# Kernel tuning notes

Measured on AMD Instinct MI355X. Metric: run time of the kernel, lower is better.

## Reference

```python
import jax, jax.numpy as jnp
import numpy as np

N_NODES = 50000
N_EDGES = 800000
IN_DIM = 128
HID = 128


def setup_inputs() -> dict:
    key = jax.random.key(0)
    ks = jax.random.split(key, 8)
    s = 1.0 / np.sqrt(IN_DIM)
    return {
        "x": jax.random.normal(ks[0], (N_NODES, IN_DIM), dtype=jnp.float32),
        "edge_index": jax.random.randint(ks[1], (2, N_EDGES), 0, N_NODES, dtype=jnp.int32),
        "W1_l": jax.random.uniform(ks[2], (HID, IN_DIM), jnp.float32, -s, s),
        "b1": jnp.zeros((HID,), jnp.float32),
        "W1_r": jax.random.uniform(ks[3], (HID, IN_DIM), jnp.float32, -s, s),
        "W2_l": jax.random.uniform(ks[4], (HID, HID), jnp.float32, -s, s),
        "b2": jnp.zeros((HID,), jnp.float32),
        "W2_r": jax.random.uniform(ks[5], (HID, HID), jnp.float32, -s, s),
    }


def _sage_conv(x, src, dst, W_l, b, W_r, n_nodes):
    # mean aggregation of source features onto destination nodes
    msg = x[src]                                    # [E, d] gather
    agg = jax.ops.segment_sum(msg, dst, num_segments=n_nodes)  # [N, d]
    deg = jax.ops.segment_sum(jnp.ones((src.shape[0],), x.dtype), dst,
                              num_segments=n_nodes)            # [N]
    agg = agg / jnp.maximum(deg, 1.0)[:, None]
    # PyG SAGEConv: lin_l(aggr) + lin_r(x_self), bias in lin_l
    return agg @ W_l.T + b + x @ W_r.T


def reference(x, edge_index, W1_l, b1, W1_r, W2_l, b2, W2_r):
    src, dst = edge_index[0], edge_index[1]
    n = x.shape[0]
    h = jax.nn.relu(_sage_conv(x, src, dst, W1_l, b1, W1_r, n))
    # dropout is identity in eval mode
    out = jax.nn.relu(_sage_conv(h, src, dst, W2_l, b2, W2_r, n))
    return out
```

## Files before the change

kernel.cpp:

```cpp
#include <hip/hip_runtime.h>

#define N_NODES 50000
#define N_EDGES 800000
#define DIM 128
#define NBINS 782
#define CAP 2048
#define EPB 8192
#define NSCAT 98

typedef _Float16 f16;
typedef _Float16 f16x4 __attribute__((ext_vector_type(4)));
typedef _Float16 f16x8 __attribute__((ext_vector_type(8)));
typedef float    f32x2 __attribute__((ext_vector_type(2)));
typedef float    f32x4 __attribute__((ext_vector_type(4)));
typedef unsigned short u16;
typedef unsigned char  u8;

__device__ inline int bucketof(int d) {
    if (d < 10) return 0;
    if (d < 13) return 1;
    if (d < 16) return 2;
    if (d < 19) return 3;
    if (d < 22) return 4;
    if (d < 26) return 5;
    if (d < 32) return 6;
    return 7;
}


__global__ __launch_bounds__(256) void k_prep(const float* __restrict__ x, u8* __restrict__ x8,
                                              const float* __restrict__ W1l, const float* __restrict__ W1r,
                                              const float* __restrict__ W2l, const float* __restrict__ W2r,
                                              f16* __restrict__ Wf1, f16* __restrict__ Wf2,
                                              int* __restrict__ binfill) {
    int b = blockIdx.x;
    if (b < 3125) {
        int idx = b * 256 + threadIdx.x;
        const float* xp = x + (size_t)idx * 8;
        float4 v0 = *(const float4*)xp;
        float4 v1 = *(const float4*)(xp + 4);
        int r0 = 0, r1 = 0;
        r0 = __builtin_amdgcn_cvt_pk_fp8_f32(v0.x, v0.y, r0, false);
        r0 = __builtin_amdgcn_cvt_pk_fp8_f32(v0.z, v0.w, r0, true);
        r1 = __builtin_amdgcn_cvt_pk_fp8_f32(v1.x, v1.y, r1, false);
        r1 = __builtin_amdgcn_cvt_pk_fp8_f32(v1.z, v1.w, r1, true);
        uint2 w; w.x = (unsigned)r0; w.y = (unsigned)r1;
        *(uint2*)(x8 + (size_t)idx * 8) = w;
    } else if (b < 3157) {
        int t = (b - 3125) * 256 + threadIdx.x;
        int layer = t >> 12;
        int nt = (t >> 9) & 7;
        int kk = (t >> 6) & 7;
        int lane = t & 63;
        int r = lane & 15, g = lane >> 4;
        int n = nt * 16 + r;
        const float* Wl_ = layer ? W2l : W1l;
        const float* Wr_ = layer ? W2r : W1r;
        f16x8 frag;
#pragma unroll
        for (int j = 0; j < 8; ++j) {
            int k = kk * 32 + g * 4 + (j & 3) + ((j >> 2) << 4);
            float f = (k < 128) ? Wl_[n * 128 + k] : Wr_[n * 128 + (k - 128)];
            frag[j] = (f16)f;
        }
        f16* dstp = (layer ? Wf2 : Wf1) + ((size_t)((nt * 8 + kk) * 64 + lane)) * 8;
        *(f16x8*)dstp = frag;
    } else {
        for (int i = threadIdx.x; i < NBINS; i += 256) binfill[i] = 0;
    }
}


__global__ __launch_bounds__(1024) void k_binscat(const int* __restrict__ src, const int* __restrict__ dst,
                                                  int* __restrict__ binfill, int* __restrict__ pairs) {
    __shared__ int hist[NBINS];
    __shared__ int base[NBINS];
    int t = threadIdx.x;
    for (int i = t; i < NBINS; i += 1024) hist[i] = 0;
    __syncthreads();
    int e0 = blockIdx.x * EPB;
    int mybin[8], myrank[8], mypack[8];
#pragma unroll
    for (int j = 0; j < 8; ++j) {
        int e = e0 + j * 1024 + t;
        if (e < N_EDGES) {
            int d = dst[e];
            int bin = d >> 6;
            mybin[j] = bin;
            mypack[j] = (src[e] << 6) | (d & 63);
            myrank[j] = atomicAdd(&hist[bin], 1);
        } else {
            mybin[j] = -1;
        }
    }
    __syncthreads();
    for (int i = t; i < NBINS; i += 1024) base[i] = atomicAdd(&binfill[i], hist[i]);
    __syncthreads();
#pragma unroll
    for (int j = 0; j < 8; ++j) {
        if (mybin[j] >= 0) {
            int bin = mybin[j];
            int pos = base[bin] + myrank[j];
            if (pos < CAP) pairs[bin * CAP + pos] = mypack[j];
        }
    }
}


__global__ __launch_bounds__(256) void k_binsolve(const int* __restrict__ pairs, const int* __restrict__ binfill,
                                                  u16* __restrict__ srt, int* __restrict__ rowbeg,
                                                  int* __restrict__ degA, int* __restrict__ order) {
    __shared__ int lcnt[64];
    __shared__ int lptr[64];
    __shared__ int lcur[64];
    __shared__ int h8[8];
    __shared__ int bb[8];
    int bin = blockIdx.x;
    int t = threadIdx.x;
    int p0 = bin * CAP;
    int cnt = min(binfill[bin], CAP);
    if (t < 64) lcnt[t] = 0;
    if (t < 8) h8[t] = 0;
    __syncthreads();
    for (int i = t; i < cnt; i += 256) atomicAdd(&lcnt[pairs[p0 + i] & 63], 1);
    __syncthreads();
    if (t < 64) {
        int d = lcnt[t];
        int v = d;
#pragma unroll
        for (int off = 1; off < 64; off <<= 1) {
            int u = __shfl_up(v, off);
            if (t >= off) v += u;
        }
        lptr[t] = v - d;
        lcur[t] = v - d;
    }
    __syncthreads();
    for (int i = t; i < cnt; i += 256) {
        int p = pairs[p0 + i];
        int slot = atomicAdd(&lcur[p & 63], 1);
        srt[p0 + slot] = (u16)(p >> 6);
    }
    int node = bin * 64 + t;
    bool act = (t < 64) && (node < N_NODES);
    int b = 0, r8 = 0;
    if (act) {
        rowbeg[node] = p0 + lptr[t];
        degA[node] = lcnt[t];
        b = bucketof(lcnt[t]);
        r8 = atomicAdd(&h8[b], 1);
    }
    __syncthreads();
    if (t == 0) {
        int r = 0;
#pragma unroll
        for (int i = 0; i < 8; ++i) { bb[i] = r; r += h8[i]; }
    }
    __syncthreads();
    if (act) order[bin * 64 + bb[b] + r8] = node;
}


__global__ __launch_bounds__(256) void k_fused(const u8* __restrict__ X8, const float* __restrict__ Xf,
                                               const f16* __restrict__ Xh16, const u16* __restrict__ srt,
                                               const int* __restrict__ rowbeg, const int* __restrict__ degA,
                                               const int* __restrict__ order, const f16* __restrict__ Wf,
                                               const float* __restrict__ bias,
                                               float* __restrict__ C, f16* __restrict__ Cb16,
                                               u8* __restrict__ Cb8) {
    __shared__ f16 agg[64][136];
    int bin = blockIdx.x;
    int n0 = bin << 6;
    int t = threadIdx.x;
    int g = t >> 4, l16 = t & 15;
    int nvalid = N_NODES - n0; if (nvalid > 64) nvalid = 64;
    const u8* __restrict__ base = X8 + l16 * 8;

#pragma unroll
    for (int p = 0; p < 4; ++p) {
        int rank = p * 16 + g;
        if (rank < nvalid) {
            int node = order[n0 + rank];
            int m = node - n0;
            int beg = rowbeg[node];
            int d = degA[node];
            int end = beg + d;
            f32x2 A0[4], A1[4], A2[4], A3[4];
#pragma unroll
            for (int j = 0; j < 4; ++j) {
                A0[j] = (f32x2){0.f, 0.f}; A1[j] = (f32x2){0.f, 0.f};
                A2[j] = (f32x2){0.f, 0.f}; A3[j] = (f32x2){0.f, 0.f};
            }
            int e = beg;
#define GACC(Ar, w) { Ar[0] += __builtin_amdgcn_cvt_pk_f32_fp8((w).x, false); \
                      Ar[1] += __builtin_amdgcn_cvt_pk_f32_fp8((w).x, true);  \
                      Ar[2] += __builtin_amdgcn_cvt_pk_f32_fp8((w).y, false); \
                      Ar[3] += __builtin_amdgcn_cvt_pk_f32_fp8((w).y, true); }
            for (; e + 4 <= end; e += 4) {
                int s0 = __builtin_nontemporal_load(srt + e);
                int s1 = __builtin_nontemporal_load(srt + e + 1);
                int s2 = __builtin_nontemporal_load(srt + e + 2);
                int s3 = __builtin_nontemporal_load(srt + e + 3);
                uint2 w0 = *(const uint2*)(base + (size_t)s0 * DIM);
                uint2 w1 = *(const uint2*)(base + (size_t)s1 * DIM);
                uint2 w2 = *(const uint2*)(base + (size_t)s2 * DIM);
                uint2 w3 = *(const uint2*)(base + (size_t)s3 * DIM);
                GACC(A0, w0); GACC(A1, w1); GACC(A2, w2); GACC(A3, w3);
            }
            if (e < end)     { uint2 w = *(const uint2*)(base + (size_t)__builtin_nontemporal_load(srt + e) * DIM); GACC(A0, w); }
            if (e + 1 < end) { uint2 w = *(const uint2*)(base + (size_t)__builtin_nontemporal_load(srt + e + 1) * DIM); GACC(A1, w); }
            if (e + 2 < end) { uint2 w = *(const uint2*)(base + (size_t)__builtin_nontemporal_load(srt + e + 2) * DIM); GACC(A2, w); }
#undef GACC
            float inv = 1.0f / fmaxf((float)d, 1.0f);
            f16x8 r;
#pragma unroll
            for (int j = 0; j < 4; ++j) {
                f32x2 s = (A0[j] + A1[j]) + (A2[j] + A3[j]);
                r[j * 2]     = (f16)(s.x * inv);
                r[j * 2 + 1] = (f16)(s.y * inv);
            }
            *(f16x8*)&agg[m][l16 * 8] = r;
        }
    }
    __syncthreads();

    int wave = t >> 6, lane = t & 63;
    int r = lane & 15, gg = lane >> 4;
    int rowloc = wave * 16 + r;
    size_t grow = (size_t)n0 + rowloc;
    size_t growc = (grow < N_NODES) ? grow : (N_NODES - 1);

    f32x4 acc[8];
#pragma unroll
    for (int nt = 0; nt < 8; ++nt) acc[nt] = (f32x4){0.f, 0.f, 0.f, 0.f};

#pragma unroll
    for (int kk = 0; kk < 8; ++kk) {
        f16x8 a;
        if (kk < 4) {
            f16x4 q0 = *(const f16x4*)&agg[rowloc][kk * 32 + gg * 4];
            f16x4 q1 = *(const f16x4*)&agg[rowloc][kk * 32 + gg * 4 + 16];
            a = __builtin_shufflevector(q0, q1, 0, 1, 2, 3, 4, 5, 6, 7);
        } else if (Xf) {
            const float* ar = Xf + growc * DIM + (kk - 4) * 32 + gg * 4;
            float4 u0 = *(const float4*)(ar);
            float4 u1 = *(const float4*)(ar + 16);
            a[0]=(f16)u0.x; a[1]=(f16)u0.y; a[2]=(f16)u0.z; a[3]=(f16)u0.w;
            a[4]=(f16)u1.x; a[5]=(f16)u1.y; a[6]=(f16)u1.z; a[7]=(f16)u1.w;
        } else {
            const f16* ar = Xh16 + growc * DIM + (kk - 4) * 32 + gg * 4;
            f16x4 q0 = *(const f16x4*)(ar);
            f16x4 q1 = *(const f16x4*)(ar + 16);
            a = __builtin_shufflevector(q0, q1, 0, 1, 2, 3, 4, 5, 6, 7);
        }
#pragma unroll
        for (int nt = 0; nt < 8; ++nt) {
            f16x8 b = *(const f16x8*)(Wf + ((size_t)((nt * 8 + kk) * 64 + lane)) * 8);
            acc[nt] = __builtin_amdgcn_mfma_f32_16x16x32_f16(a, b, acc[nt], 0, 0, 0);
        }
    }
    size_t rbase = (size_t)n0 + wave * 16 + gg * 4;
#pragma unroll
    for (int nt = 0; nt < 8; ++nt) {
        int colc = nt * 16 + r;
        float bv = bias[colc];
#pragma unroll
        for (int q = 0; q < 4; ++q) {
            size_t node = rbase + q;
            if (node < N_NODES) {
                float v = fmaxf(acc[nt][q] + bv, 0.f);
                if (C)    C[node * DIM + colc] = v;
                if (Cb16) Cb16[node * DIM + colc] = (f16)v;
                if (Cb8) {
                    int pk = __builtin_amdgcn_cvt_pk_fp8_f32(v, v, 0, false);
                    Cb8[node * DIM + colc] = (u8)(pk & 0xff);
                }
            }
        }
    }
}


extern "C" void kernel_launch(void* const* d_in, const int* in_sizes, int n_in,
                              void* d_out, int out_size, void* d_ws, size_t ws_size,
                              hipStream_t stream) {
    const float* x   = (const float*)d_in[0];
    const int*   ei  = (const int*)d_in[1];
    const float* W1l = (const float*)d_in[2];
    const float* b1  = (const float*)d_in[3];
    const float* W1r = (const float*)d_in[4];
    const float* W2l = (const float*)d_in[5];
    const float* b2  = (const float*)d_in[6];
    const float* W2r = (const float*)d_in[7];
    float* out = (float*)d_out;

    const int* src = ei;
    const int* dst = ei + N_EDGES;

    char* ws = (char*)d_ws;
    int*  binfill = (int*)(ws + 0);
    int*  degA    = (int*)(ws + 3200);
    int*  rowbeg  = (int*)(ws + 203264);
    int*  order   = (int*)(ws + 403264);
    u16*  srt     = (u16*)(ws + 603264);
    u8*   x8      = (u8*)(ws + 3806336);
    f16*  hh      = (f16*)(ws + 10206336);
    int*  pairs   = (int*)(ws + 23006336);
    u8*   hh8     = (u8*)(ws + 23006336);
    f16*  Wf1     = (f16*)(ws + 29412480);
    f16*  Wf2     = Wf1 + 32768;

    dim3 blk(256);
    k_prep<<<dim3(3158), blk, 0, stream>>>(x, x8, W1l, W1r, W2l, W2r, Wf1, Wf2, binfill);
    k_binscat<<<dim3(NSCAT), dim3(1024), 0, stream>>>(src, dst, binfill, pairs);
    k_binsolve<<<dim3(NBINS), blk, 0, stream>>>(pairs, binfill, srt, rowbeg, degA, order);

    k_fused<<<dim3(NBINS), blk, 0, stream>>>(x8, x, (const f16*)nullptr, srt, rowbeg, degA, order,
                                             Wf1, b1, (float*)nullptr, hh, hh8);

    k_fused<<<dim3(NBINS), blk, 0, stream>>>(hh8, (const float*)nullptr, hh, srt, rowbeg, degA, order,
                                             Wf2, b2, out, (f16*)nullptr, (u8*)nullptr);
}
```

Before: 120.1 us.

## Merge edge binning scatter into prep kernel and drop nontemporal index loads

The separate 1024-thread binning scatter kernel is folded into the prep kernel as extra 256-thread blocks, so x quantization, weight packing and edge binning run concurrently in one launch. A tiny zeroing kernel is added to clear the bin counters beforehand. The scatter now does two passes over dst (histogram, then re-read with fresh ranks) instead of keeping ranks in registers, which costs extra reads and atomics. Separately, the neighbor index loads in the gather loop become regular loads instead of nontemporal ones.

After: 138.6 us. +15.4%, slower.

```diff
diff --git a/kernel.cpp b/kernel.cpp
--- a/kernel.cpp
+++ b/kernel.cpp
@@ -28,11 +28,18 @@
 }
 
 
-__global__ __launch_bounds__(256) void k_prep(const float* __restrict__ x, u8* __restrict__ x8,
-                                              const float* __restrict__ W1l, const float* __restrict__ W1r,
-                                              const float* __restrict__ W2l, const float* __restrict__ W2r,
-                                              f16* __restrict__ Wf1, f16* __restrict__ Wf2,
-                                              int* __restrict__ binfill) {
+__global__ __launch_bounds__(256) void k_zero(int* __restrict__ p) {
+    int i = blockIdx.x * 256 + threadIdx.x;
+    if (i < NBINS) p[i] = 0;
+}
+
+
+__global__ __launch_bounds__(256) void k_prepscat(const float* __restrict__ x, u8* __restrict__ x8,
+                                                  const float* __restrict__ W1l, const float* __restrict__ W1r,
+                                                  const float* __restrict__ W2l, const float* __restrict__ W2r,
+                                                  f16* __restrict__ Wf1, f16* __restrict__ Wf2,
+                                                  const int* __restrict__ src, const int* __restrict__ dst,
+                                                  int* __restrict__ binfill, int* __restrict__ pairs) {
     int b = blockIdx.x;
     if (b < 3125) {
         int idx = b * 256 + threadIdx.x;
@@ -66,42 +73,32 @@
         f16* dstp = (layer ? Wf2 : Wf1) + ((size_t)((nt * 8 + kk) * 64 + lane)) * 8;
         *(f16x8*)dstp = frag;
     } else {
-        for (int i = threadIdx.x; i < NBINS; i += 256) binfill[i] = 0;
-    }
-}
-
-
-__global__ __launch_bounds__(1024) void k_binscat(const int* __restrict__ src, const int* __restrict__ dst,
-                                                  int* __restrict__ binfill, int* __restrict__ pairs) {
-    __shared__ int hist[NBINS];
-    __shared__ int base[NBINS];
-    int t = threadIdx.x;
-    for (int i = t; i < NBINS; i += 1024) hist[i] = 0;
-    __syncthreads();
-    int e0 = blockIdx.x * EPB;
-    int mybin[8], myrank[8], mypack[8];
-#pragma unroll
-    for (int j = 0; j < 8; ++j) {
-        int e = e0 + j * 1024 + t;
-        if (e < N_EDGES) {
-            int d = dst[e];
-            int bin = d >> 6;
-            mybin[j] = bin;
-            mypack[j] = (src[e] << 6) | (d & 63);
-            myrank[j] = atomicAdd(&hist[bin], 1);
-        } else {
-            mybin[j] = -1;
-        }
-    }
-    __syncthreads();
-    for (int i = t; i < NBINS; i += 1024) base[i] = atomicAdd(&binfill[i], hist[i]);
-    __syncthreads();
-#pragma unroll
-    for (int j = 0; j < 8; ++j) {
-        if (mybin[j] >= 0) {
-            int bin = mybin[j];
-            int pos = base[bin] + myrank[j];
-            if (pos < CAP) pairs[bin * CAP + pos] = mypack[j];
+        __shared__ int hist[NBINS];
+        __shared__ int base[NBINS];
+        int t = threadIdx.x;
+        int e0 = (b - 3157) * EPB;
+        for (int i = t; i < NBINS; i += 256) hist[i] = 0;
+        __syncthreads();
+#pragma unroll 4
+        for (int j = 0; j < 32; ++j) {
+            int e = e0 + j * 256 + t;
+            if (e < N_EDGES) atomicAdd(&hist[dst[e] >> 6], 1);
+        }
+        __syncthreads();
+        for (int i = t; i < NBINS; i += 256) base[i] = atomicAdd(&binfill[i], hist[i]);
+        __syncthreads();
+        for (int i = t; i < NBINS; i += 256) hist[i] = 0;
+        __syncthreads();
+#pragma unroll 4
+        for (int j = 0; j < 32; ++j) {
+            int e = e0 + j * 256 + t;
+            if (e < N_EDGES) {
+                int d = dst[e];
+                int bin = d >> 6;
+                int rk = atomicAdd(&hist[bin], 1);
+                int pos = base[bin] + rk;
+                if (pos < CAP) pairs[bin * CAP + pos] = (src[e] << 6) | (d & 63);
+            }
         }
     }
 }
@@ -197,19 +194,19 @@
                       Ar[2] += __builtin_amdgcn_cvt_pk_f32_fp8((w).y, false); \
                       Ar[3] += __builtin_amdgcn_cvt_pk_f32_fp8((w).y, true); }
             for (; e + 4 <= end; e += 4) {
-                int s0 = __builtin_nontemporal_load(srt + e);
-                int s1 = __builtin_nontemporal_load(srt + e + 1);
-                int s2 = __builtin_nontemporal_load(srt + e + 2);
-                int s3 = __builtin_nontemporal_load(srt + e + 3);
+                int s0 = srt[e];
+                int s1 = srt[e + 1];
+                int s2 = srt[e + 2];
+                int s3 = srt[e + 3];
                 uint2 w0 = *(const uint2*)(base + (size_t)s0 * DIM);
                 uint2 w1 = *(const uint2*)(base + (size_t)s1 * DIM);
                 uint2 w2 = *(const uint2*)(base + (size_t)s2 * DIM);
                 uint2 w3 = *(const uint2*)(base + (size_t)s3 * DIM);
                 GACC(A0, w0); GACC(A1, w1); GACC(A2, w2); GACC(A3, w3);
             }
-            if (e < end)     { uint2 w = *(const uint2*)(base + (size_t)__builtin_nontemporal_load(srt + e) * DIM); GACC(A0, w); }
-            if (e + 1 < end) { uint2 w = *(const uint2*)(base + (size_t)__builtin_nontemporal_load(srt + e + 1) * DIM); GACC(A1, w); }
-            if (e + 2 < end) { uint2 w = *(const uint2*)(base + (size_t)__builtin_nontemporal_load(srt + e + 2) * DIM); GACC(A2, w); }
+            if (e < end)     { uint2 w = *(const uint2*)(base + (size_t)srt[e] * DIM); GACC(A0, w); }
+            if (e + 1 < end) { uint2 w = *(const uint2*)(base + (size_t)srt[e + 1] * DIM); GACC(A1, w); }
+            if (e + 2 < end) { uint2 w = *(const uint2*)(base + (size_t)srt[e + 2] * DIM); GACC(A2, w); }
 #undef GACC
             float inv = 1.0f / fmaxf((float)d, 1.0f);
             f16x8 r;
@@ -311,8 +308,9 @@
     f16*  Wf2     = Wf1 + 32768;
 
     dim3 blk(256);
-    k_prep<<<dim3(3158), blk, 0, stream>>>(x, x8, W1l, W1r, W2l, W2r, Wf1, Wf2, binfill);
-    k_binscat<<<dim3(NSCAT), dim3(1024), 0, stream>>>(src, dst, binfill, pairs);
+    k_zero<<<dim3(4), blk, 0, stream>>>(binfill);
+    k_prepscat<<<dim3(3255), blk, 0, stream>>>(x, x8, W1l, W1r, W2l, W2r, Wf1, Wf2,
+                                               src, dst, binfill, pairs);
     k_binsolve<<<dim3(NBINS), blk, 0, stream>>>(pairs, binfill, srt, rowbeg, degA, order);
 
     k_fused<<<dim3(NBINS), blk, 0, stream>>>(x8, x, (const f16*)nullptr, srt, rowbeg, degA, order,
```
